# Optimization experiments

Measured on AMD Instinct MI355X. Metric: run time of the kernel, lower is better.

## Reference

```python
import jax, jax.numpy as jnp
import numpy as np

E, L, M, F, S, P = 4, 10, 512, 128, 1000, 10  # envs, labels, max_sample, features, sample_size, batch_len


def setup_inputs() -> dict:
    key = jax.random.key(0)
    k1, k2, k3 = jax.random.split(key, 3)
    data_len = jax.random.randint(k1, (E, L), M // 2, M + 1, dtype=jnp.int32)
    matrix = jax.random.normal(k2, (E, L, M, F), dtype=jnp.float32)
    # zero out padded samples beyond data_len (as shape_to_matrix does)
    pad_mask = jnp.arange(M)[None, None, :, None] < data_len[:, :, None, None]
    matrix = matrix * pad_mask
    params = jnp.eye(F, dtype=jnp.float32) + 0.01 * jax.random.normal(k3, (F, F), dtype=jnp.float32)
    is_train_env = jnp.array([True, True, False, False])
    return {"matrix": matrix, "params": params, "data_len": data_len, "is_train_env": is_train_env}


def reference(matrix, params, data_len, is_train_env):
    lenf = data_len.astype(matrix.dtype)  # [E,L], torch keeps this as float32
    # __init__ preprocessing: normalize by mean std over sample dim (detached in torch)
    std = jax.lax.stop_gradient(jnp.std(matrix, axis=2).mean())
    mat = matrix / std
    # Silverman-style bandwidth on the normalized matrix (detached in torch)
    bw = jax.lax.stop_gradient(1.06 * (M ** (-1.0 / 5.0)) * jnp.std(mat, axis=2).mean())
    offset = jnp.exp(-0.5 / bw ** 2)
    proj = jnp.einsum('elmf,fg->elmg', mat, params)  # [E,L,M,F]
    left = jax.lax.stop_gradient(proj.min())   # .item() in torch -> constant
    right = jax.lax.stop_gradient(proj.max())
    delta = (right - left) / S
    x_grid = jnp.linspace(left, right, S)
    divisor = jnp.sqrt(2.0 * jnp.pi) * bw

    def step(acc, points):  # points: [P] grid chunk
        d2 = (proj[..., None] - points) ** 2                     # [E,L,M,F,P]
        s = jnp.sum(offset ** d2, axis=2)                        # [E,L,F,P]
        # remove contribution of zero-padded samples, then normalize by true count
        corr = (M - lenf)[:, :, None] * (offset ** (points ** 2))[None, None, :]  # [E,L,P]
        r = (s - corr[:, :, None, :]) / lenf[:, :, None, None]   # [E,L,F,P]
        d = jnp.sum(jnp.abs(r[:, None] - r[None, :]), axis=-1)   # [E,E,L,F] pairwise L1 over grid chunk
        return acc + d, None

    store_dis, _ = jax.lax.scan(step, jnp.zeros((E, E, L, F), proj.dtype), x_grid.reshape(S // P, P))
    store_dis = store_dis / divisor  # [E,E,L,F]

    idx = jnp.arange(E)
    upper = idx[:, None] < idx[None, :]                                   # all env pairs i<j
    train_pair = upper & is_train_env[:, None] & is_train_env[None, :]    # train env pairs i<j
    half = store_dis * (delta / 2.0)
    neg = jnp.array(-jnp.inf, half.dtype)
    test_results = jnp.where(upper[:, :, None, None], half, neg).max(axis=(0, 1))        # [L,F]
    train_results = jnp.where(train_pair[:, :, None, None], half, neg).max(axis=(0, 1))  # [L,F]
    train_dis = train_results.max(axis=0).mean()
    test_dis = test_results.max(axis=0).mean()
    return train_results, test_results, train_dis, test_dis
```

## Files before the change

### kernel.cpp

```cpp
#include <hip/hip_runtime.h>
#include <cmath>

#define E_ 4
#define L_ 10
#define M_ 512
#define F_ 128
#define S_ 1000

typedef unsigned int u32;
typedef _Float16 f16;
typedef __attribute__((ext_vector_type(8))) _Float16 v8h;
typedef __attribute__((ext_vector_type(4))) float v4f;

__device__ __forceinline__ float fexp2(float a){
#if __has_builtin(__builtin_amdgcn_exp2f)
  return __builtin_amdgcn_exp2f(a);
#else
  return exp2f(a);
#endif
}


__global__ __launch_bounds__(256) void k_pre(const float* __restrict__ mat,
                       const float* __restrict__ par,
                       float* __restrict__ projT, float* __restrict__ wsf){
  __shared__ float sm[512];
  int b = blockIdx.x, tid = threadIdx.x;
  if (b >= 1280){
    int el = b - 1280;
    int f = tid & 127, part = tid >> 7;
    const float* base = mat + ((size_t)el * M_ + part*256) * F_;
    float s = 0.f, s2 = 0.f;
    for (int i = 0; i < 256; i++){
      float v = base[i*F_ + f];
      s += v; s2 += v*v;
    }
    sm[tid] = s; sm[256 + tid] = s2;
    __syncthreads();
    if (tid < 128){
      wsf[2576 + el*128 + tid] = sm[tid] + sm[tid+128];
      wsf[7696 + el*128 + tid] = sm[256+tid] + sm[256+tid+128];
    }
    return;
  }
  int el = b >> 5, mt = (b & 31) * 16;
  int lane = tid & 63, wave = tid >> 6;
  int q = (lane >> 4) & 3, m16 = lane & 15;
  const float* arow = mat + ((size_t)el * M_ + mt + m16) * F_;
  v4f acc0 = {0.f,0.f,0.f,0.f}, acc1 = {0.f,0.f,0.f,0.f};
  #pragma unroll
  for (int c = 0; c < 4; c++){
    float4 a0 = *(const float4*)&arow[c*32 + q*8];
    float4 a1 = *(const float4*)&arow[c*32 + q*8 + 4];
    v8h af, b0, b1;
    af[0]=(f16)a0.x; af[1]=(f16)a0.y; af[2]=(f16)a0.z; af[3]=(f16)a0.w;
    af[4]=(f16)a1.x; af[5]=(f16)a1.y; af[6]=(f16)a1.z; af[7]=(f16)a1.w;
    const float* pb = par + (c*32 + q*8)*F_ + wave*32 + m16;
    #pragma unroll
    for (int j = 0; j < 8; j++){
      b0[j] = (f16)pb[j*F_];
      b1[j] = (f16)pb[j*F_ + 16];
    }
    acc0 = __builtin_amdgcn_mfma_f32_16x16x32_f16(af, b0, acc0, 0, 0, 0);
    acc1 = __builtin_amdgcn_mfma_f32_16x16x32_f16(af, b1, acc1, 0, 0, 0);
  }
  *(float4*)(projT + ((size_t)el*F_ + wave*32      + m16)*M_ + mt + q*4)
      = make_float4(acc0[0], acc0[1], acc0[2], acc0[3]);
  *(float4*)(projT + ((size_t)el*F_ + wave*32 + 16 + m16)*M_ + mt + q*4)
      = make_float4(acc1[0], acc1[1], acc1[2], acc1[3]);
  float lmin =  3.4e38f, lmax = -3.4e38f;
  #pragma unroll
  for (int r = 0; r < 4; r++){
    lmin = fminf(lmin, fminf(acc0[r], acc1[r]));
    lmax = fmaxf(lmax, fmaxf(acc0[r], acc1[r]));
  }
  #pragma unroll
  for (int d = 32; d >= 1; d >>= 1){
    lmin = fminf(lmin, __shfl_xor(lmin, d, 64));
    lmax = fmaxf(lmax, __shfl_xor(lmax, d, 64));
  }
  if (lane == 0){ sm[wave] = lmin; sm[8+wave] = lmax; }
  __syncthreads();
  if (tid == 0){
    wsf[16   + b] = fminf(fminf(sm[0], sm[1]), fminf(sm[2], sm[3]));
    wsf[1296 + b] = fmaxf(fmaxf(sm[8], sm[9]), fmaxf(sm[10], sm[11]));
  }
}

__global__ __launch_bounds__(256) void k_kde(const float* __restrict__ projT,
                      const int* __restrict__ dlen, float* __restrict__ wsf,
                      float* __restrict__ dpair, float k2c, float divisor){
  __shared__ __align__(16) float smem[5104];
  int b = blockIdx.x;
  int l = b >> 7, f = b & 127;
  int tid = threadIdx.x, wave = tid >> 6, lane = tid & 63;
  for (int idx = tid; idx < 512; idx += 256){
    int e = idx >> 7, mq = idx & 127;
    ((float4*)smem)[idx] =
      ((const float4*)(projT + (((size_t)e * L_ + l) * F_ + f) * M_))[mq];
  }
  float mn = 3.4e38f, mx = -3.4e38f, s = 0.f;
  for (int i = tid; i < 1280; i += 256){
    mn = fminf(mn, wsf[16   + i]);
    mx = fmaxf(mx, wsf[1296 + i]);
  }
  for (int i = tid; i < 5120; i += 256){
    float a  = wsf[2576 + i];
    float a2 = wsf[7696 + i];
    float mean = a * (1.0f/512.0f);
    float var  = a2 * (1.0f/512.0f) - mean*mean;
    s += sqrtf(fmaxf(var, 0.0f));
  }
  smem[2048+tid] = mn; smem[2304+tid] = mx; smem[2560+tid] = s;
  __syncthreads();
  for (int g = 128; g >= 1; g >>= 1){
    if (tid < g){
      smem[2048+tid] = fminf(smem[2048+tid], smem[2048+tid+g]);
      smem[2304+tid] = fmaxf(smem[2304+tid], smem[2304+tid+g]);
      smem[2560+tid] += smem[2560+tid+g];
    }
    __syncthreads();
  }
  if (tid == 0){
    float rstd   = 5120.0f / smem[2560];
    float leftS  = smem[2048] * rstd;
    float rightS = smem[2304] * rstd;
    float stepFS = (rightS - leftS) * (1.0f/999.0f);
    float inv2   = 1.0f / (2.0f * stepFS);
    smem[5072] = rstd * inv2;
    smem[5073] = leftS * inv2;
    smem[5074] = stepFS;
    smem[5075] = leftS;
    if (b == 0)
      wsf[8] = ((rightS - leftS) * (1.0f/1000.0f)) * 0.5f / divisor;
  }
  __syncthreads();
  float posScale = smem[5072], posOff = smem[5073];
  float stepFS = smem[5074], leftS = smem[5075];
  __syncthreads();
  for (int idx = tid; idx < 656; idx += 256)
    ((float4*)(smem + 2048))[idx] = make_float4(0.f,0.f,0.f,0.f);
  float sh = 2.0f * stepFS;
  if (tid < 72){
    int u = tid - 34;
    float d0 = (float)(2*u)   * sh;
    float d1 = (float)(2*u-1) * sh;
    float2 t = (tid < 69) ? make_float2(fexp2(k2c*d0*d0), fexp2(k2c*d1*d1))
                          : make_float2(0.f, 0.f);
    *(float2*)&smem[4672 + 2*tid] = t;
  }
  {
    float xc = fmaf((float)(tid - 1), 4.0f*stepFS, leftS);
    smem[4816 + tid] = fexp2(k2c * xc * xc);
  }
  __syncthreads();
  {
    float* hf = smem + 2048 + wave*656;
    const float4* spw4 = (const float4*)(smem + wave*512);
    float4 p0 = spw4[lane], p1 = spw4[lane + 64];
    float pv[8] = {p0.x,p0.y,p0.z,p0.w,p1.x,p1.y,p1.z,p1.w};
    #pragma unroll
    for (int i = 0; i < 8; i++){
      float pos = fmaf(pv[i], posScale, -posOff);
      float n = floorf(pos + 0.5f);
      float d = pos - n;
      float wm = 0.5f*(0.5f-d)*(0.5f-d);
      float wp = 0.5f*(0.5f+d)*(0.5f+d);
      float w0 = 0.75f - d*d;
      int base = (int)n + 71;
      atomicAdd(&hf[base  ], wm);
      atomicAdd(&hf[base+1], w0);
      atomicAdd(&hf[base+2], wp);
    }
  }
  __syncthreads();
  float lenE = (float)dlen[wave*L_ + l];
  float rlen = 1.0f / lenE;
  float padc = 512.0f - lenE;
  {
    const float* sK = smem + 4672;
    const float* hb = smem + 2048 + wave*656;
    float a0=0.f, a1=0.f, a2=0.f, a3=0.f;
    #pragma unroll 8
    for (int uu = 0; uu < 72; uu++){
      float2 kv = *(const float2*)&sK[2*uu];
      int off = 2*(69 - uu) + 2*lane;
      float2 h0 = *(const float2*)&hb[off];
      float2 h1 = *(const float2*)&hb[off + 128];
      float2 h2 = *(const float2*)&hb[off + 256];
      float2 h3 = *(const float2*)&hb[off + 384];
      a0 = fmaf(h0.x, kv.x, fmaf(h0.y, kv.y, a0));
      a1 = fmaf(h1.x, kv.x, fmaf(h1.y, kv.y, a1));
      a2 = fmaf(h2.x, kv.x, fmaf(h2.y, kv.y, a2));
      a3 = fmaf(h3.x, kv.x, fmaf(h3.y, kv.y, a3));
    }
    const float* sCorr = smem + 4816;
    smem[wave*256 + lane      ] = (a0 - padc * sCorr[lane      ]) * rlen;
    smem[wave*256 + lane +  64] = (a1 - padc * sCorr[lane +  64]) * rlen;
    smem[wave*256 + lane + 128] = (a2 - padc * sCorr[lane + 128]) * rlen;
    smem[wave*256 + lane + 192] = (a3 - padc * sCorr[lane + 192]) * rlen;
  }
  __syncthreads();
  float ps[6] = {0,0,0,0,0,0};
  #pragma unroll
  for (int r=0;r<4;r++){
    int t = tid + 256*r;
    if (t < S_){
      int cc = t >> 2;
      float u = (float)(t & 3) * 0.25f;
      float um1 = u - 1.0f, um2 = u - 2.0f, up1 = u + 1.0f;
      float w0 = -u * um1 * um2 * (1.0f/6.0f);
      float w1 = up1 * um1 * um2 * 0.5f;
      float w2 = -u * up1 * um2 * 0.5f;
      float w3 = u * up1 * um1 * (1.0f/6.0f);
      float rr[4];
      #pragma unroll
      for (int e=0;e<4;e++){
        const float* st = &smem[e*256 + cc];
        rr[e] = w0*st[0] + w1*st[1] + w2*st[2] + w3*st[3];
      }
      ps[0] += fabsf(rr[0]-rr[1]);
      ps[1] += fabsf(rr[0]-rr[2]);
      ps[2] += fabsf(rr[0]-rr[3]);
      ps[3] += fabsf(rr[1]-rr[2]);
      ps[4] += fabsf(rr[1]-rr[3]);
      ps[5] += fabsf(rr[2]-rr[3]);
    }
  }
  #pragma unroll
  for (int pr=0; pr<6; pr++){
    float v = ps[pr];
    #pragma unroll
    for (int d=32; d>=1; d>>=1) v += __shfl_xor(v, d, 64);
    if (lane == 0) smem[5072 + wave*8 + pr] = v;
  }
  __syncthreads();
  if (tid < 6)
    dpair[tid*1280 + b] = smem[5072+tid] + smem[5080+tid] + smem[5088+tid] + smem[5096+tid];
}

__global__ void k_fin(const float* __restrict__ dpair, const float* __restrict__ wsf,
                      const int* __restrict__ istrain, float* __restrict__ out){
  __shared__ float str[1280], ste[1280];
  __shared__ float s1[128], s2[128];
  int tid = threadIdx.x;
  float hscale = wsf[8];
  bool t0 = istrain[0]!=0, t1 = istrain[1]!=0, t2 = istrain[2]!=0, t3 = istrain[3]!=0;
  bool trn[6] = { t0&&t1, t0&&t2, t0&&t3, t1&&t2, t1&&t3, t2&&t3 };
  for (int idx = tid; idx < 1280; idx += 256){
    float tmax = -INFINITY, trmax = -INFINITY;
    #pragma unroll
    for (int pr=0;pr<6;pr++){
      float h = dpair[pr*1280 + idx] * hscale;
      tmax = fmaxf(tmax, h);
      if (trn[pr]) trmax = fmaxf(trmax, h);
    }
    out[idx]        = trmax;
    out[1280 + idx] = tmax;
    str[idx] = trmax; ste[idx] = tmax;
  }
  __syncthreads();
  if (tid < 128){
    float m1 = -INFINITY, m2 = -INFINITY;
    for (int l=0;l<L_;l++){
      m1 = fmaxf(m1, str[l*F_ + tid]);
      m2 = fmaxf(m2, ste[l*F_ + tid]);
    }
    s1[tid] = m1; s2[tid] = m2;
  }
  __syncthreads();
  for (int g=64; g>=1; g>>=1){
    if (tid < g){ s1[tid] += s1[tid+g]; s2[tid] += s2[tid+g]; }
    __syncthreads();
  }
  if (tid == 0){
    out[2560] = s1[0] * (1.0f/128.0f);
    out[2561] = s2[0] * (1.0f/128.0f);
  }
}

extern "C" void kernel_launch(void* const* d_in, const int* in_sizes, int n_in,
                              void* d_out, int out_size, void* d_ws, size_t ws_size,
                              hipStream_t stream){
  const float* mat = (const float*)d_in[0];
  const float* par = (const float*)d_in[1];
  const int*  dlen = (const int*)d_in[2];
  const int*  istr = (const int*)d_in[3];
  float* out   = (float*)d_out;
  float* wsf   = (float*)d_ws;
  float* dpair = wsf + 12816;
  float* projT = wsf + 20496;

  double bw_d   = 1.06 * pow(512.0, -0.2);
  float  bw     = (float)bw_d;
  float  offset = expf(-0.5f / (bw*bw));
  float  k2c    = (float)(log((double)offset) * 1.4426950408889634);
  float  divisor = sqrtf(6.283185307179586f) * bw;

  k_pre <<<1320, 256, 0, stream>>>(mat, par, projT, wsf);
  k_kde <<<1280, 256, 0, stream>>>(projT, dlen, wsf, dpair, k2c, divisor);
  k_fin <<<1,    256, 0, stream>>>(dpair, wsf, istr, out);
}
```

Baseline: 158.3 us.

## Fuse final reduction into KDE kernel and use atomics for global min/max/std

k_pre now reduces the per-column std and the projection min/max into a few global words using order-preserving integer atomics, instead of writing thousands of partials. k_kde no longer has each of its 1280 blocks re-reduce those partials. k_kde loads projections straight into registers rather than staging them through shared memory, and trims the kernel-tap loop from 72 to 64. It also folds in the k_fin work through atomicMax per feature and a last-block-done counter, which removes one kernel launch. In exchange it adds two memset calls and atomic contention, and the narrower tap window slightly changes the numerical truncation.

```diff
diff --git a/kernel.cpp b/kernel.cpp
--- a/kernel.cpp
+++ b/kernel.cpp
@@ -18,6 +18,14 @@
 #else
   return exp2f(a);
 #endif
+}
+
+__device__ __forceinline__ u32 fenc(float f){
+  u32 u = __float_as_uint(f);
+  return (u & 0x80000000u) ? ~u : (u | 0x80000000u);
+}
+__device__ __forceinline__ float fdec(u32 k){
+  return __uint_as_float((k & 0x80000000u) ? (k ^ 0x80000000u) : ~k);
 }
 
 
@@ -38,9 +46,18 @@
     sm[tid] = s; sm[256 + tid] = s2;
     __syncthreads();
     if (tid < 128){
-      wsf[2576 + el*128 + tid] = sm[tid] + sm[tid+128];
-      wsf[7696 + el*128 + tid] = sm[256+tid] + sm[256+tid+128];
-    }
+      float a1 = sm[tid] + sm[tid+128];
+      float a2 = sm[256+tid] + sm[384+tid];
+      float mean = a1 * (1.0f/512.0f);
+      float var  = a2 * (1.0f/512.0f) - mean*mean;
+      sm[tid] = sqrtf(fmaxf(var, 0.0f));
+    }
+    __syncthreads();
+    for (int g = 64; g >= 1; g >>= 1){
+      if (tid < g) sm[tid] += sm[tid+g];
+      __syncthreads();
+    }
+    if (tid == 0) wsf[272 + el] = sm[0];
     return;
   }
   int el = b >> 5, mt = (b & 31) * 16;
@@ -82,82 +99,53 @@
   if (lane == 0){ sm[wave] = lmin; sm[8+wave] = lmax; }
   __syncthreads();
   if (tid == 0){
-    wsf[16   + b] = fminf(fminf(sm[0], sm[1]), fminf(sm[2], sm[3]));
-    wsf[1296 + b] = fmaxf(fmaxf(sm[8], sm[9]), fmaxf(sm[10], sm[11]));
+    float mn = fminf(fminf(sm[0], sm[1]), fminf(sm[2], sm[3]));
+    float mx = fmaxf(fmaxf(sm[8], sm[9]), fmaxf(sm[10], sm[11]));
+    atomicMin(&((u32*)wsf)[264], fenc(mn));
+    atomicMax(&((u32*)wsf)[0],   fenc(mx));
   }
 }
 
 __global__ __launch_bounds__(256) void k_kde(const float* __restrict__ projT,
-                      const int* __restrict__ dlen, float* __restrict__ wsf,
-                      float* __restrict__ dpair, float k2c, float divisor){
-  __shared__ __align__(16) float smem[5104];
+                      const int* __restrict__ dlen, const int* __restrict__ istr,
+                      float* __restrict__ wsf, float* __restrict__ out,
+                      float k2c, float divisor){
+  __shared__ __align__(16) float smem[4064];
+  __shared__ int sflag;
   int b = blockIdx.x;
   int l = b >> 7, f = b & 127;
   int tid = threadIdx.x, wave = tid >> 6, lane = tid & 63;
-  for (int idx = tid; idx < 512; idx += 256){
-    int e = idx >> 7, mq = idx & 127;
-    ((float4*)smem)[idx] =
-      ((const float4*)(projT + (((size_t)e * L_ + l) * F_ + f) * M_))[mq];
-  }
-  float mn = 3.4e38f, mx = -3.4e38f, s = 0.f;
-  for (int i = tid; i < 1280; i += 256){
-    mn = fminf(mn, wsf[16   + i]);
-    mx = fmaxf(mx, wsf[1296 + i]);
-  }
-  for (int i = tid; i < 5120; i += 256){
-    float a  = wsf[2576 + i];
-    float a2 = wsf[7696 + i];
-    float mean = a * (1.0f/512.0f);
-    float var  = a2 * (1.0f/512.0f) - mean*mean;
-    s += sqrtf(fmaxf(var, 0.0f));
-  }
-  smem[2048+tid] = mn; smem[2304+tid] = mx; smem[2560+tid] = s;
-  __syncthreads();
-  for (int g = 128; g >= 1; g >>= 1){
-    if (tid < g){
-      smem[2048+tid] = fminf(smem[2048+tid], smem[2048+tid+g]);
-      smem[2304+tid] = fmaxf(smem[2304+tid], smem[2304+tid+g]);
-      smem[2560+tid] += smem[2560+tid+g];
-    }
-    __syncthreads();
-  }
-  if (tid == 0){
-    float rstd   = 5120.0f / smem[2560];
-    float leftS  = smem[2048] * rstd;
-    float rightS = smem[2304] * rstd;
-    float stepFS = (rightS - leftS) * (1.0f/999.0f);
-    float inv2   = 1.0f / (2.0f * stepFS);
-    smem[5072] = rstd * inv2;
-    smem[5073] = leftS * inv2;
-    smem[5074] = stepFS;
-    smem[5075] = leftS;
-    if (b == 0)
-      wsf[8] = ((rightS - leftS) * (1.0f/1000.0f)) * 0.5f / divisor;
-  }
-  __syncthreads();
-  float posScale = smem[5072], posOff = smem[5073];
-  float stepFS = smem[5074], leftS = smem[5075];
-  __syncthreads();
+  u32* wsu = (u32*)wsf;
+  const float4* col = (const float4*)(projT + (((size_t)wave * L_ + l) * F_ + f) * M_);
+  float4 p0 = col[lane], p1 = col[lane + 64];
+  float mx = fdec(wsu[0]);
+  float mn = fdec(wsu[264]);
+  float ssum = 0.f;
+  #pragma unroll
+  for (int j = 0; j < 40; j++) ssum += wsf[272 + j];
+  float rstd   = 5120.0f / ssum;
+  float leftS  = mn * rstd, rightS = mx * rstd;
+  float stepFS = (rightS - leftS) * (1.0f/999.0f);
+  float inv2   = 1.0f / (2.0f * stepFS);
+  float posScale = rstd * inv2, posOff = leftS * inv2;
+  float hscale = ((rightS - leftS) * (1.0f/1000.0f)) * 0.5f / divisor;
   for (int idx = tid; idx < 656; idx += 256)
-    ((float4*)(smem + 2048))[idx] = make_float4(0.f,0.f,0.f,0.f);
+    ((float4*)(smem + 1024))[idx] = make_float4(0.f,0.f,0.f,0.f);
   float sh = 2.0f * stepFS;
-  if (tid < 72){
-    int u = tid - 34;
+  if (tid < 64){
+    int u = tid - 32;
     float d0 = (float)(2*u)   * sh;
     float d1 = (float)(2*u-1) * sh;
-    float2 t = (tid < 69) ? make_float2(fexp2(k2c*d0*d0), fexp2(k2c*d1*d1))
-                          : make_float2(0.f, 0.f);
-    *(float2*)&smem[4672 + 2*tid] = t;
+    *(float2*)&smem[3648 + 2*tid] =
+        make_float2(fexp2(k2c*d0*d0), fexp2(k2c*d1*d1));
   }
   {
     float xc = fmaf((float)(tid - 1), 4.0f*stepFS, leftS);
-    smem[4816 + tid] = fexp2(k2c * xc * xc);
+    smem[3776 + tid] = fexp2(k2c * xc * xc);
   }
   __syncthreads();
   {
-    float* hf = smem + 2048 + wave*656;
-    const float4* spw4 = (const float4*)(smem + wave*512);
-    float4 p0 = spw4[lane], p1 = spw4[lane + 64];
+    float* hf = smem + 1024 + wave*656;
     float pv[8] = {p0.x,p0.y,p0.z,p0.w,p1.x,p1.y,p1.z,p1.w};
     #pragma unroll
     for (int i = 0; i < 8; i++){
@@ -178,13 +166,13 @@
   float rlen = 1.0f / lenE;
   float padc = 512.0f - lenE;
   {
-    const float* sK = smem + 4672;
-    const float* hb = smem + 2048 + wave*656;
+    const float* sK = smem + 3648;
+    const float* hb = smem + 1024 + wave*656;
     float a0=0.f, a1=0.f, a2=0.f, a3=0.f;
     #pragma unroll 8
-    for (int uu = 0; uu < 72; uu++){
+    for (int uu = 0; uu < 64; uu++){
       float2 kv = *(const float2*)&sK[2*uu];
-      int off = 2*(69 - uu) + 2*lane;
+      int off = 2*(67 - uu) + 2*lane;
       float2 h0 = *(const float2*)&hb[off];
       float2 h1 = *(const float2*)&hb[off + 128];
       float2 h2 = *(const float2*)&hb[off + 256];
@@ -194,7 +182,7 @@
       a2 = fmaf(h2.x, kv.x, fmaf(h2.y, kv.y, a2));
       a3 = fmaf(h3.x, kv.x, fmaf(h3.y, kv.y, a3));
     }
-    const float* sCorr = smem + 4816;
+    const float* sCorr = smem + 3776;
     smem[wave*256 + lane      ] = (a0 - padc * sCorr[lane      ]) * rlen;
     smem[wave*256 + lane +  64] = (a1 - padc * sCorr[lane +  64]) * rlen;
     smem[wave*256 + lane + 128] = (a2 - padc * sCorr[lane + 128]) * rlen;
@@ -232,50 +220,43 @@
     float v = ps[pr];
     #pragma unroll
     for (int d=32; d>=1; d>>=1) v += __shfl_xor(v, d, 64);
-    if (lane == 0) smem[5072 + wave*8 + pr] = v;
-  }
-  __syncthreads();
-  if (tid < 6)
-    dpair[tid*1280 + b] = smem[5072+tid] + smem[5080+tid] + smem[5088+tid] + smem[5096+tid];
-}
-
-__global__ void k_fin(const float* __restrict__ dpair, const float* __restrict__ wsf,
-                      const int* __restrict__ istrain, float* __restrict__ out){
-  __shared__ float str[1280], ste[1280];
-  __shared__ float s1[128], s2[128];
-  int tid = threadIdx.x;
-  float hscale = wsf[8];
-  bool t0 = istrain[0]!=0, t1 = istrain[1]!=0, t2 = istrain[2]!=0, t3 = istrain[3]!=0;
-  bool trn[6] = { t0&&t1, t0&&t2, t0&&t3, t1&&t2, t1&&t3, t2&&t3 };
-  for (int idx = tid; idx < 1280; idx += 256){
+    if (lane == 0) smem[4032 + wave*8 + pr] = v;
+  }
+  __syncthreads();
+  if (tid == 0){
+    bool t0 = istr[0]!=0, t1 = istr[1]!=0, t2 = istr[2]!=0, t3 = istr[3]!=0;
+    bool trn[6] = { t0&&t1, t0&&t2, t0&&t3, t1&&t2, t1&&t3, t2&&t3 };
     float tmax = -INFINITY, trmax = -INFINITY;
     #pragma unroll
     for (int pr=0;pr<6;pr++){
-      float h = dpair[pr*1280 + idx] * hscale;
+      float h = (smem[4032+pr] + smem[4040+pr] + smem[4048+pr] + smem[4056+pr]) * hscale;
       tmax = fmaxf(tmax, h);
       if (trn[pr]) trmax = fmaxf(trmax, h);
     }
-    out[idx]        = trmax;
-    out[1280 + idx] = tmax;
-    str[idx] = trmax; ste[idx] = tmax;
-  }
-  __syncthreads();
-  if (tid < 128){
-    float m1 = -INFINITY, m2 = -INFINITY;
-    for (int l=0;l<L_;l++){
-      m1 = fmaxf(m1, str[l*F_ + tid]);
-      m2 = fmaxf(m2, ste[l*F_ + tid]);
-    }
-    s1[tid] = m1; s2[tid] = m2;
-  }
-  __syncthreads();
-  for (int g=64; g>=1; g>>=1){
-    if (tid < g){ s1[tid] += s1[tid+g]; s2[tid] += s2[tid+g]; }
+    out[b]        = trmax;
+    out[1280 + b] = tmax;
+    atomicMax(&wsu[2   + f], fenc(trmax));
+    atomicMax(&wsu[130 + f], fenc(tmax));
+    __threadfence();
+    u32 old = atomicAdd(&wsu[1], 1u);
+    sflag = (old == 1279u);
+  }
+  __syncthreads();
+  if (sflag){
+    __threadfence();
+    if (tid < 128){
+      smem[tid]       = fdec(atomicOr(&wsu[2   + tid], 0u));
+      smem[128 + tid] = fdec(atomicOr(&wsu[130 + tid], 0u));
+    }
     __syncthreads();
-  }
-  if (tid == 0){
-    out[2560] = s1[0] * (1.0f/128.0f);
-    out[2561] = s2[0] * (1.0f/128.0f);
+    for (int g = 64; g >= 1; g >>= 1){
+      if (tid < g){ smem[tid] += smem[tid+g]; smem[128+tid] += smem[128+tid+g]; }
+      __syncthreads();
+    }
+    if (tid == 0){
+      out[2560] = smem[0]   * (1.0f/128.0f);
+      out[2561] = smem[128] * (1.0f/128.0f);
+    }
   }
 }
 
@@ -286,10 +267,9 @@
   const float* par = (const float*)d_in[1];
   const int*  dlen = (const int*)d_in[2];
   const int*  istr = (const int*)d_in[3];
-  float* out   = (float*)d_out;
-  float* wsf   = (float*)d_ws;
-  float* dpair = wsf + 12816;
-  float* projT = wsf + 20496;
+  float* out = (float*)d_out;
+  float* wsf = (float*)d_ws;
+  float* projT = wsf + 512;
 
   double bw_d   = 1.06 * pow(512.0, -0.2);
   float  bw     = (float)bw_d;
@@ -297,7 +277,9 @@
   float  k2c    = (float)(log((double)offset) * 1.4426950408889634);
   float  divisor = sqrtf(6.283185307179586f) * bw;
 
+  hipMemsetAsync(wsf, 0, 1056, stream);
+  hipMemsetAsync((char*)wsf + 1056, 0xFF, 4, stream);
+
   k_pre <<<1320, 256, 0, stream>>>(mat, par, projT, wsf);
-  k_kde <<<1280, 256, 0, stream>>>(projT, dlen, wsf, dpair, k2c, divisor);
-  k_fin <<<1,    256, 0, stream>>>(dpair, wsf, istr, out);
-}
+  k_kde <<<1280, 256, 0, stream>>>(projT, dlen, istr, wsf, out, k2c, divisor);
+}
```

Result: slower. 164.6 us (+4.0%).
